# Optimization experiments

Hardware: AMD Instinct MI355X
Metric: run time of the kernel (lower is better)

Reference implementation:

```python
import math
import jax, jax.numpy as jnp
import numpy as np

B, C, T = 4, 512, 1024
H = 8
KC = C // H
WIN = 4


def _get_relative_embeddings(emb, length):
    win = (emb.shape[1] - 1) // 2
    pad_length = max(length - (win + 1), 0)
    slice_start = max(win + 1 - length, 0)
    slice_end = slice_start + 2 * length - 1
    if pad_length > 0:
        emb = jnp.pad(emb, ((0, 0), (pad_length, pad_length), (0, 0)))
    return emb[:, slice_start:slice_end]


def _relative_to_absolute(x):
    # x: [b, h, L, 2L-1] -> [b, h, L, L] via skew trick
    b, h, L, _ = x.shape
    x = jnp.pad(x, ((0, 0), (0, 0), (0, 0), (0, 1)))          # [b,h,L,2L]
    x_flat = x.reshape(b, h, L * 2 * L)
    x_flat = jnp.pad(x_flat, ((0, 0), (0, 0), (0, L - 1)))    # [b,h,(L+1)(2L-1)]
    x_final = x_flat.reshape(b, h, L + 1, 2 * L - 1)
    return x_final[:, :, :L, L - 1:]


def _absolute_to_relative(x):
    # x: [b, h, L, L] -> [b, h, L, 2L-1]
    b, h, L, _ = x.shape
    x = jnp.pad(x, ((0, 0), (0, 0), (0, 0), (0, L - 1)))      # [b,h,L,2L-1]
    x_flat = x.reshape(b, h, L * (2 * L - 1))
    x_flat = jnp.pad(x_flat, ((0, 0), (0, 0), (L, 0)))        # [b,h,2L^2]
    x_final = x_flat.reshape(b, h, L, 2 * L)
    return x_final[:, :, :, 1:]


def setup_inputs() -> dict:
    key = jax.random.key(0)
    ks = jax.random.split(key, 12)
    xavier = math.sqrt(6.0 / (C + C))  # xavier_uniform for [C, C, 1] conv weight
    rel_std = KC ** (-0.5)
    return {
        "x": jax.random.normal(ks[0], (B, C, T), dtype=jnp.float32),
        "wq": jax.random.uniform(ks[1], (C, C), jnp.float32, -xavier, xavier),
        "bq": jnp.zeros((C,), jnp.float32),
        "wk": jax.random.uniform(ks[2], (C, C), jnp.float32, -xavier, xavier),
        "bk": jnp.zeros((C,), jnp.float32),
        "wv": jax.random.uniform(ks[3], (C, C), jnp.float32, -xavier, xavier),
        "bv": jnp.zeros((C,), jnp.float32),
        "wo": jax.random.normal(ks[4], (C, C), jnp.float32) * (1.0 / math.sqrt(C)),
        "bo": jnp.zeros((C,), jnp.float32),
        "emb_rel_k": jax.random.normal(ks[5], (1, 2 * WIN + 1, KC), jnp.float32) * rel_std,
        "emb_rel_v": jax.random.normal(ks[6], (1, 2 * WIN + 1, KC), jnp.float32) * rel_std,
    }


def reference(x, wq, bq, wk, bk, wv, bv, wo, bo, emb_rel_k, emb_rel_v):
    b, c, t = x.shape
    # 1x1 conv == channel matmul
    q = jnp.einsum("oi,bit->bot", wq, x) + bq[:, None]
    k = jnp.einsum("oi,bit->bot", wk, x) + bk[:, None]
    v = jnp.einsum("oi,bit->bot", wv, x) + bv[:, None]
    # [b, H, t, kc]
    q = q.reshape(b, H, KC, t).transpose(0, 1, 3, 2)
    k = k.reshape(b, H, KC, t).transpose(0, 1, 3, 2)
    v = v.reshape(b, H, KC, t).transpose(0, 1, 3, 2)
    inv_sqrt = 1.0 / math.sqrt(KC)
    scores = jnp.einsum("bhtc,bhsc->bhts", q, k) * inv_sqrt
    rel_k = _get_relative_embeddings(emb_rel_k, t)[0]            # [2t-1, kc]
    rel_logits = jnp.einsum("bhtc,rc->bhtr", q, rel_k)           # [b,h,t,2t-1]
    scores = scores + _relative_to_absolute(rel_logits) * inv_sqrt
    p_attn = jax.nn.softmax(scores, axis=-1)
    output = jnp.einsum("bhts,bhsc->bhtc", p_attn, v)
    rel_weights = _absolute_to_relative(p_attn)                  # [b,h,t,2t-1]
    rel_v = _get_relative_embeddings(emb_rel_v, t)[0]            # [2t-1, kc]
    output = output + jnp.einsum("bhtr,rc->bhtc", rel_weights, rel_v)
    output = output.transpose(0, 1, 3, 2).reshape(b, c, t)
    return jnp.einsum("oi,bit->bot", wo, output) + bo[:, None]
```

## Files before the change

### kernel.cpp

```cpp
#include <hip/hip_runtime.h>
#include <hip/hip_bf16.h>

#define Bdim 4
#define Cdim 512
#define Tdim 1024
#define Hn   8
#define KCd  64

typedef __attribute__((ext_vector_type(8))) short bf16x8;
typedef __attribute__((ext_vector_type(4))) float f32x4;

__device__ __forceinline__ unsigned short f32_bf16_rne(float f) {
    unsigned u = __float_as_uint(f);
    u += 0x7FFFu + ((u >> 16) & 1u);
    return (unsigned short)(u >> 16);
}
__device__ __forceinline__ float bf16_f32(unsigned short h) {
    return __uint_as_float(((unsigned)h) << 16);
}
__device__ __forceinline__ void split8(const float* f, bf16x8& h8, bf16x8& l8) {
    #pragma unroll
    for (int e = 0; e < 8; ++e) {
        const unsigned short hh = f32_bf16_rne(f[e]);
        h8[e] = (short)hh;
        l8[e] = (short)f32_bf16_rne(f[e] - bf16_f32(hh));
    }
}

__device__ __forceinline__ int sw(int row, int col) {
    return (row << 6) + ((((col >> 3) ^ (row & 7)) << 3) | (col & 7));
}
__device__ __forceinline__ bf16x8 fragld(const unsigned short* a, int row, int kstep, int quad) {
    return *(const bf16x8*)&a[(row << 6) + ((((kstep << 2) | quad) ^ (row & 7)) << 3)];
}


__global__ __launch_bounds__(256) void prep_kernel(
    const float* __restrict__ wq, const float* __restrict__ wk,
    const float* __restrict__ wv, const float* __restrict__ wo,
    const float* __restrict__ x,
    unsigned short* __restrict__ WAhi, unsigned short* __restrict__ WAlo,
    unsigned short* __restrict__ XBhi, unsigned short* __restrict__ XBlo)
{
    const int w = threadIdx.x >> 6, lane = threadIdx.x & 63;
    const int l15 = lane & 15, quad = lane >> 4;
    const int task = blockIdx.x * 4 + w;

    if (task < 2048) {
        const int mtile = task >> 4, kt = task & 15;
        const int sel = mtile >> 5;
        const float* W = sel == 0 ? wq : (sel == 1 ? wk : (sel == 2 ? wv : wo));
        const int row = (mtile & 31) * 16 + l15;
        const float* p = W + (size_t)row * Cdim + kt * 32 + quad * 8;
        float f[8];
        *(float4*)&f[0] = *(const float4*)p;
        *(float4*)&f[4] = *(const float4*)(p + 4);
        bf16x8 h8, l8;
        split8(f, h8, l8);
        const size_t base = (size_t)task * 512 + lane * 8;
        *(bf16x8*)(WAhi + base) = h8;
        *(bf16x8*)(WAlo + base) = l8;
    } else {
        const int t2 = task - 2048;
        const int b = t2 >> 10, ntile = (t2 >> 4) & 63, kt = t2 & 15;
        const float* Xb = x + (size_t)b * Cdim * Tdim;
        const int n = ntile * 16 + l15;
        const int k0 = kt * 32 + quad * 8;
        float f[8];
        #pragma unroll
        for (int e = 0; e < 8; ++e) f[e] = Xb[(size_t)(k0 + e) * Tdim + n];
        bf16x8 h8, l8;
        split8(f, h8, l8);
        const size_t base = (size_t)t2 * 512 + lane * 8;
        *(bf16x8*)(XBhi + base) = h8;
        *(bf16x8*)(XBlo + base) = l8;
    }
}

__global__ __launch_bounds__(256, 3) void gemm_qkv(
    const unsigned short* __restrict__ Ahi, const unsigned short* __restrict__ Alo,
    const unsigned short* __restrict__ Bhi, const unsigned short* __restrict__ Blo,
    const float* __restrict__ bq, const float* __restrict__ bk, const float* __restrict__ bv,
    unsigned short* __restrict__ qhi, unsigned short* __restrict__ qlo,
    unsigned short* __restrict__ khi, unsigned short* __restrict__ klo,
    unsigned short* __restrict__ vhi, unsigned short* __restrict__ vlo)
{
    const int tid = threadIdx.x;
    const int w = tid >> 6, lane = tid & 63;
    const int l15 = lane & 15, quad = lane >> 4;
    const int lo8 = lane << 3;

    const int id = blockIdx.x;
    const int xcd = id & 7, slot = id >> 3;
    const int col = xcd * 16 + slot / 6;
    const int mg  = slot % 6;
    const int b = col >> 5, n32 = col & 31;
    const int m64 = mg * 4 + w;
    const int sel = m64 >> 3;
    const int mtb = m64 * 4;
    const int ntb = b * 64 + n32 * 2;

    f32x4 acc[4][2];
    #pragma unroll
    for (int i = 0; i < 4; ++i)
        #pragma unroll
        for (int j = 0; j < 2; ++j) acc[i][j] = (f32x4){0.f, 0.f, 0.f, 0.f};

    bf16x8 Ah[2][4], Al[2][4], Bh[2][2], Bl[2][2];
    #pragma unroll
    for (int mt = 0; mt < 4; ++mt) {
        const size_t o = (size_t)(mtb + mt) * 8192 + lo8;
        Ah[0][mt] = *(const bf16x8*)(Ahi + o);
        Al[0][mt] = *(const bf16x8*)(Alo + o);
    }
    #pragma unroll
    for (int nt = 0; nt < 2; ++nt) {
        const size_t o = (size_t)(ntb + nt) * 8192 + lo8;
        Bh[0][nt] = *(const bf16x8*)(Bhi + o);
        Bl[0][nt] = *(const bf16x8*)(Blo + o);
    }

    for (int kt = 0; kt < 16; ++kt) {
        const int cur = kt & 1, nxt = cur ^ 1;
        if (kt < 15) {
            const int kn = (kt + 1) * 512;
            #pragma unroll
            for (int mt = 0; mt < 4; ++mt) {
                const size_t o = (size_t)(mtb + mt) * 8192 + kn + lo8;
                Ah[nxt][mt] = *(const bf16x8*)(Ahi + o);
                Al[nxt][mt] = *(const bf16x8*)(Alo + o);
            }
            #pragma unroll
            for (int nt = 0; nt < 2; ++nt) {
                const size_t o = (size_t)(ntb + nt) * 8192 + kn + lo8;
                Bh[nxt][nt] = *(const bf16x8*)(Bhi + o);
                Bl[nxt][nt] = *(const bf16x8*)(Blo + o);
            }
        }
        #pragma unroll
        for (int mt = 0; mt < 4; ++mt)
            #pragma unroll
            for (int nt = 0; nt < 2; ++nt) {
                f32x4 c = acc[mt][nt];
                c = __builtin_amdgcn_mfma_f32_16x16x32_bf16(Ah[cur][mt], Bh[cur][nt], c, 0, 0, 0);
                c = __builtin_amdgcn_mfma_f32_16x16x32_bf16(Ah[cur][mt], Bl[cur][nt], c, 0, 0, 0);
                c = __builtin_amdgcn_mfma_f32_16x16x32_bf16(Al[cur][mt], Bh[cur][nt], c, 0, 0, 0);
                acc[mt][nt] = c;
            }
    }

    const int head = m64 & 7;
    const size_t hbase = ((size_t)(b * Hn + head) * 16) << 12;
    if (sel < 2) {
        const float* Bv = sel == 0 ? bq : bk;
        unsigned short* ph = sel == 0 ? qhi : khi;
        unsigned short* pl = sel == 0 ? qlo : klo;
        #pragma unroll
        for (int mt = 0; mt < 4; ++mt) {
            const int c0 = mt * 16 + quad * 4;
            float bb[4];
            #pragma unroll
            for (int r = 0; r < 4; ++r) bb[r] = Bv[head * 64 + c0 + r];
            const int lane_out = (((c0 >> 3) & 3) << 4) + l15;
            const int e0 = c0 & 7;
            const int cg = c0 >> 5;
            #pragma unroll
            for (int nt = 0; nt < 2; ++nt) {
                const int tile = n32 >> 1;
                const int rhi = (n32 & 1) * 2 + nt;
                const int g = rhi * 2 + cg;
                const size_t off = hbase + ((size_t)tile << 12) + g * 512
                                 + (size_t)lane_out * 8 + e0;
                ushort4 h4, l4;
                #pragma unroll
                for (int r = 0; r < 4; ++r) {
                    const float v = acc[mt][nt][r] + bb[r];
                    const unsigned short hh = f32_bf16_rne(v);
                    ((unsigned short*)&h4)[r] = hh;
                    ((unsigned short*)&l4)[r] = f32_bf16_rne(v - bf16_f32(hh));
                }
                *(ushort4*)(ph + off) = h4;
                *(ushort4*)(pl + off) = l4;
            }
        }
    } else {
        #pragma unroll
        for (int mt = 0; mt < 4; ++mt) {
            const int c0 = mt * 16 + quad * 4;
            float bb[4];
            #pragma unroll
            for (int r = 0; r < 4; ++r) bb[r] = bv[head * 64 + c0 + r];
            #pragma unroll
            for (int nt = 0; nt < 2; ++nt) {
                const int t = n32 * 32 + nt * 16 + l15;
                const int tile = t >> 6, jl = t & 63;
                const int jg = jl >> 5, lanej = ((jl >> 3) & 3) << 4;
                const int e = jl & 7;
                const size_t tb = hbase + ((size_t)tile << 12);
                #pragma unroll
                for (int r = 0; r < 4; ++r) {
                    const int c = c0 + r;
                    const int g = mt * 2 + jg;
                    const int lane_v = lanej + (c & 15);
                    const float v = acc[mt][nt][r] + bb[r];
                    const unsigned short hh = f32_bf16_rne(v);
                    const size_t off = tb + g * 512 + (size_t)lane_v * 8 + e;
                    vhi[off] = hh;
                    vlo[off] = f32_bf16_rne(v - bf16_f32(hh));
                }
            }
        }
    }
}

__global__ __launch_bounds__(256) void gemm_out(
    const unsigned short* __restrict__ Ahi, const unsigned short* __restrict__ Alo,
    const unsigned short* __restrict__ Bhi, const unsigned short* __restrict__ Blo,
    const float* __restrict__ bo, float* __restrict__ out)
{
    const int tid = threadIdx.x;
    const int w = tid >> 6, lane = tid & 63;
    const int l15 = lane & 15, quad = lane >> 4;
    const int lo8 = lane << 3;

    const int id = blockIdx.x;
    const int xcd = id & 7, slot = id >> 3;
    const int col = xcd * 16 + (slot >> 2);
    const int mg  = slot & 3;
    const int b = col >> 5, n32 = col & 31;
    const int m32 = mg * 4 + w;
    const int mtb = 96 + m32 * 2;
    const int ntb = b * 64 + n32 * 2;

    f32x4 acc[2][2];
    #pragma unroll
    for (int i = 0; i < 2; ++i)
        #pragma unroll
        for (int j = 0; j < 2; ++j) acc[i][j] = (f32x4){0.f, 0.f, 0.f, 0.f};

    bf16x8 Ah[2][2], Al[2][2], Bh[2][2], Bl[2][2];
    #pragma unroll
    for (int mt = 0; mt < 2; ++mt) {
        const size_t o = (size_t)(mtb + mt) * 8192 + lo8;
        Ah[0][mt] = *(const bf16x8*)(Ahi + o);
        Al[0][mt] = *(const bf16x8*)(Alo + o);
    }
    #pragma unroll
    for (int nt = 0; nt < 2; ++nt) {
        const size_t o = (size_t)(ntb + nt) * 8192 + lo8;
        Bh[0][nt] = *(const bf16x8*)(Bhi + o);
        Bl[0][nt] = *(const bf16x8*)(Blo + o);
    }

    for (int kt = 0; kt < 16; ++kt) {
        const int cur = kt & 1, nxt = cur ^ 1;
        if (kt < 15) {
            const int kn = (kt + 1) * 512;
            #pragma unroll
            for (int mt = 0; mt < 2; ++mt) {
                const size_t o = (size_t)(mtb + mt) * 8192 + kn + lo8;
                Ah[nxt][mt] = *(const bf16x8*)(Ahi + o);
                Al[nxt][mt] = *(const bf16x8*)(Alo + o);
            }
            #pragma unroll
            for (int nt = 0; nt < 2; ++nt) {
                const size_t o = (size_t)(ntb + nt) * 8192 + kn + lo8;
                Bh[nxt][nt] = *(const bf16x8*)(Bhi + o);
                Bl[nxt][nt] = *(const bf16x8*)(Blo + o);
            }
        }
        #pragma unroll
        for (int mt = 0; mt < 2; ++mt)
            #pragma unroll
            for (int nt = 0; nt < 2; ++nt) {
                f32x4 c = acc[mt][nt];
                c = __builtin_amdgcn_mfma_f32_16x16x32_bf16(Ah[cur][mt], Bh[cur][nt], c, 0, 0, 0);
                c = __builtin_amdgcn_mfma_f32_16x16x32_bf16(Ah[cur][mt], Bl[cur][nt], c, 0, 0, 0);
                c = __builtin_amdgcn_mfma_f32_16x16x32_bf16(Al[cur][mt], Bh[cur][nt], c, 0, 0, 0);
                acc[mt][nt] = c;
            }
    }

    float* Ob = out + (size_t)b * Cdim * Tdim;
    #pragma unroll
    for (int mt = 0; mt < 2; ++mt) {
        const int m = m32 * 32 + mt * 16 + quad * 4;
        float bb[4];
        #pragma unroll
        for (int r = 0; r < 4; ++r) bb[r] = bo[m + r];
        #pragma unroll
        for (int nt = 0; nt < 2; ++nt) {
            const int t = n32 * 32 + nt * 16 + l15;
            #pragma unroll
            for (int r = 0; r < 4; ++r)
                Ob[(size_t)(m + r) * Tdim + t] = acc[mt][nt][r] + bb[r];
        }
    }
}

__global__ __launch_bounds__(256) void attn_mfma(
    const unsigned short* __restrict__ qhi, const unsigned short* __restrict__ qlo,
    const unsigned short* __restrict__ khi, const unsigned short* __restrict__ klo,
    const unsigned short* __restrict__ vhi, const unsigned short* __restrict__ vlo,
    const float* __restrict__ ek,
    const float* __restrict__ ev,
    unsigned short* __restrict__ cxhi, unsigned short* __restrict__ cxlo)
{
    __shared__ alignas(16) unsigned short psh[4096], psl[4096];
    __shared__ float rk[576];
    __shared__ float evs[576];

    const int tid = threadIdx.x;
    int it, h, b;
    {
        const int n = blockIdx.x;
        const int xcd = n & 7, slot = n >> 3;
        const int pair = (xcd << 2) | (slot >> 4);
        it = slot & 15;
        b = pair >> 3;
        h = pair & 7;
    }
    const int i0 = it * 64;
    const int lane = tid & 63, w = tid >> 6;
    const int l15 = lane & 15, quad = lane >> 4;
    const int m_blk = w * 16 + l15;
    const int lo8 = lane << 3;

    const size_t bh16 = (size_t)(b * Hn + h) * 16;

    bf16x8 qfh[2], qfl[2];
    {
        const unsigned short* qth = qhi + ((bh16 + it) << 12);
        const unsigned short* qtl = qlo + ((bh16 + it) << 12);
        #pragma unroll
        for (int ks = 0; ks < 2; ++ks) {
            qfh[ks] = *(const bf16x8*)(qth + (((w << 1) | ks) << 9) + lo8);
            qfl[ks] = *(const bf16x8*)(qtl + (((w << 1) | ks) << 9) + lo8);
        }
    }

    bf16x8 ekh[2], ekl[2];
    #pragma unroll
    for (int ks = 0; ks < 2; ++ks) {
        #pragma unroll
        for (int j = 0; j < 8; ++j) { ekh[ks][j] = 0; ekl[ks][j] = 0; }
        if (l15 < 9) {
            #pragma unroll
            for (int j = 0; j < 8; ++j) {
                const float v = ek[l15 * 64 + ks * 32 + quad * 8 + j];
                const unsigned short hh = f32_bf16_rne(v);
                ekh[ks][j] = (short)hh;
                ekl[ks][j] = (short)f32_bf16_rne(v - bf16_f32(hh));
            }
        }
    }

    {
        f32x4 rkD = (f32x4){0.f, 0.f, 0.f, 0.f};
        #pragma unroll
        for (int ks = 0; ks < 2; ++ks) {
            rkD = __builtin_amdgcn_mfma_f32_16x16x32_bf16(qfh[ks], ekh[ks], rkD, 0, 0, 0);
            rkD = __builtin_amdgcn_mfma_f32_16x16x32_bf16(qfh[ks], ekl[ks], rkD, 0, 0, 0);
            rkD = __builtin_amdgcn_mfma_f32_16x16x32_bf16(qfl[ks], ekh[ks], rkD, 0, 0, 0);
        }
        if (l15 < 9) {
            #pragma unroll
            for (int r = 0; r < 4; ++r)
                rk[(w * 16 + quad * 4 + r) * 9 + l15] = rkD[r];
        }
    }
    for (int idx = tid; idx < 576; idx += 256) evs[idx] = ev[idx];
    __syncthreads();

    float m_run = -1e30f, l_run = 0.f;
    f32x4 Oc[4];
    #pragma unroll
    for (int ct = 0; ct < 4; ++ct) Oc[ct] = (f32x4){0.f, 0.f, 0.f, 0.f};

    const unsigned short* kh0 = khi + (bh16 << 12);
    const unsigned short* kl0 = klo + (bh16 << 12);
    const unsigned short* vh0 = vhi + (bh16 << 12);
    const unsigned short* vl0 = vlo + (bh16 << 12);

    for (int t = 0; t < 16; ++t) {
        const int j0 = t << 6;
        const size_t tb = (size_t)t << 12;
        const unsigned short* kht = kh0 + tb;
        const unsigned short* klt = kl0 + tb;
        const unsigned short* vht = vh0 + tb;
        const unsigned short* vlt = vl0 + tb;

        bf16x8 vbh[2][4], vbl[2][4];
        #pragma unroll
        for (int ks = 0; ks < 2; ++ks)
            #pragma unroll
            for (int ct = 0; ct < 4; ++ct) {
                vbh[ks][ct] = *(const bf16x8*)(vht + (((ct << 1) | ks) << 9) + lo8);
                vbl[ks][ct] = *(const bf16x8*)(vlt + (((ct << 1) | ks) << 9) + lo8);
            }

        f32x4 Sc[4];
        #pragma unroll
        for (int jt = 0; jt < 4; ++jt) Sc[jt] = (f32x4){0.f, 0.f, 0.f, 0.f};
        #pragma unroll
        for (int ks = 0; ks < 2; ++ks) {
            bf16x8 ah[4], al[4];
            #pragma unroll
            for (int jt = 0; jt < 4; ++jt) {
                ah[jt] = *(const bf16x8*)(kht + (((jt << 1) | ks) << 9) + lo8);
                al[jt] = *(const bf16x8*)(klt + (((jt << 1) | ks) << 9) + lo8);
            }
            #pragma unroll
            for (int jt = 0; jt < 4; ++jt) {
                Sc[jt] = __builtin_amdgcn_mfma_f32_16x16x32_bf16(ah[jt], qfh[ks], Sc[jt], 0, 0, 0);
                Sc[jt] = __builtin_amdgcn_mfma_f32_16x16x32_bf16(ah[jt], qfl[ks], Sc[jt], 0, 0, 0);
                Sc[jt] = __builtin_amdgcn_mfma_f32_16x16x32_bf16(al[jt], qfh[ks], Sc[jt], 0, 0, 0);
            }
        }

        const int dt = j0 - i0;
        const bool diag = (dt >= -67 && dt <= 67);
        if (diag) {
            #pragma unroll
            for (int jt = 0; jt < 4; ++jt) {
                const int db = dt + jt * 16 + quad * 4 - m_blk;
                #pragma unroll
                for (int r = 0; r < 4; ++r) {
                    const int d = db + r;
                    if ((unsigned)(d + 4) <= 8u) Sc[jt][r] += rk[m_blk * 9 + d + 4];
                }
            }
        }

        float mt = -1e30f;
        #pragma unroll
        for (int jt = 0; jt < 4; ++jt)
            #pragma unroll
            for (int r = 0; r < 4; ++r) {
                Sc[jt][r] *= 0.125f;
                mt = fmaxf(mt, Sc[jt][r]);
            }
        mt = fmaxf(mt, __shfl_xor(mt, 16));
        mt = fmaxf(mt, __shfl_xor(mt, 32));
        const float mn = fmaxf(m_run, mt);
        const float alpha = __expf(m_run - mn);
        float rs = 0.f;
        #pragma unroll
        for (int jt = 0; jt < 4; ++jt)
            #pragma unroll
            for (int r = 0; r < 4; ++r) {
                const float e = __expf(Sc[jt][r] - mn);
                Sc[jt][r] = e;
                rs += e;
            }
        rs += __shfl_xor(rs, 16);
        rs += __shfl_xor(rs, 32);
        l_run = l_run * alpha + rs;
        m_run = mn;

        #pragma unroll
        for (int jt = 0; jt < 4; ++jt) {
            ushort4 ph, pl;
            ph.x = f32_bf16_rne(Sc[jt][0]); pl.x = f32_bf16_rne(Sc[jt][0] - bf16_f32(ph.x));
            ph.y = f32_bf16_rne(Sc[jt][1]); pl.y = f32_bf16_rne(Sc[jt][1] - bf16_f32(ph.y));
            ph.z = f32_bf16_rne(Sc[jt][2]); pl.z = f32_bf16_rne(Sc[jt][2] - bf16_f32(ph.z));
            ph.w = f32_bf16_rne(Sc[jt][3]); pl.w = f32_bf16_rne(Sc[jt][3] - bf16_f32(ph.w));
            const int o = sw(m_blk, jt * 16 + quad * 4);
            *(ushort4*)&psh[o] = ph;
            *(ushort4*)&psl[o] = pl;
        }

        const float al0 = __shfl(alpha, quad * 4 + 0);
        const float al1 = __shfl(alpha, quad * 4 + 1);
        const float al2 = __shfl(alpha, quad * 4 + 2);
        const float al3 = __shfl(alpha, quad * 4 + 3);
        #pragma unroll
        for (int ct = 0; ct < 4; ++ct) {
            Oc[ct][0] *= al0; Oc[ct][1] *= al1; Oc[ct][2] *= al2; Oc[ct][3] *= al3;
        }
        #pragma unroll
        for (int ks = 0; ks < 2; ++ks) {
            bf16x8 pah = fragld(psh, m_blk, ks, quad);
            bf16x8 pal = fragld(psl, m_blk, ks, quad);
            #pragma unroll
            for (int ct = 0; ct < 4; ++ct) {
                Oc[ct] = __builtin_amdgcn_mfma_f32_16x16x32_bf16(pah, vbh[ks][ct], Oc[ct], 0, 0, 0);
                Oc[ct] = __builtin_amdgcn_mfma_f32_16x16x32_bf16(pah, vbl[ks][ct], Oc[ct], 0, 0, 0);
                Oc[ct] = __builtin_amdgcn_mfma_f32_16x16x32_bf16(pal, vbh[ks][ct], Oc[ct], 0, 0, 0);
            }
        }

        if (diag) {
            #pragma unroll
            for (int r = 0; r < 4; ++r) {
                const int mrow = w * 16 + quad * 4 + r;
                const int ig = i0 + mrow;
                #pragma unroll
                for (int e = 0; e < 9; ++e) {
                    const int jl = ig + e - 4 - j0;
                    if ((unsigned)jl < 64u) {
                        const int o = sw(mrow, jl);
                        const float p = bf16_f32(psh[o]) + bf16_f32(psl[o]);
                        #pragma unroll
                        for (int ct = 0; ct < 4; ++ct)
                            Oc[ct][r] += p * evs[e * 64 + ct * 16 + l15];
                    }
                }
            }
        }
    }

    const float rlv = 1.f / l_run;
    float rl[4];
    rl[0] = __shfl(rlv, quad * 4 + 0);
    rl[1] = __shfl(rlv, quad * 4 + 1);
    rl[2] = __shfl(rlv, quad * 4 + 2);
    rl[3] = __shfl(rlv, quad * 4 + 3);
    const int ntile16 = it * 4 + w;
    const int e = l15 & 7;
    #pragma unroll
    for (int ct = 0; ct < 4; ++ct) {
        const int cl = ct * 16 + l15;
        const int ktc = h * 2 + (cl >> 5);
        const int lane_c = (((ct * 2 + (l15 >> 3)) & 3) << 4) + quad * 4;
        const size_t base = (((size_t)(b * 64 + ntile16)) * 16 + ktc) * 512;
        #pragma unroll
        for (int r = 0; r < 4; ++r) {
            const float v = Oc[ct][r] * rl[r];
            const unsigned short hh = f32_bf16_rne(v);
            const size_t off = base + (size_t)(lane_c + r) * 8 + e;
            cxhi[off] = hh;
            cxlo[off] = f32_bf16_rne(v - bf16_f32(hh));
        }
    }
}

extern "C" void kernel_launch(void* const* d_in, const int* in_sizes, int n_in,
                              void* d_out, int out_size, void* d_ws, size_t ws_size,
                              hipStream_t stream) {
    const float* x  = (const float*)d_in[0];
    const float* wq = (const float*)d_in[1];
    const float* bq = (const float*)d_in[2];
    const float* wk = (const float*)d_in[3];
    const float* bk = (const float*)d_in[4];
    const float* wv = (const float*)d_in[5];
    const float* bv = (const float*)d_in[6];
    const float* wo = (const float*)d_in[7];
    const float* bo = (const float*)d_in[8];
    const float* ek = (const float*)d_in[9];
    const float* ev = (const float*)d_in[10];
    float* out = (float*)d_out;

    const size_t PW = 2048u * 512u;
    const size_t PX = 4u * 1024u * 512u;
    unsigned short* WAhi = (unsigned short*)d_ws;
    unsigned short* WAlo = WAhi + PW;
    unsigned short* XBhi = WAlo + PW;
    unsigned short* XBlo = XBhi + PX;
    unsigned short* qhi  = XBlo + PX;
    unsigned short* qlo  = qhi + PX;
    unsigned short* khi  = qlo + PX;
    unsigned short* klo  = khi + PX;
    unsigned short* vhi  = klo + PX;
    unsigned short* vlo  = vhi + PX;
    unsigned short* cxhi = vlo + PX;
    unsigned short* cxlo = cxhi + PX;

    prep_kernel<<<dim3(1536), 256, 0, stream>>>(
        wq, wk, wv, wo, x, WAhi, WAlo, XBhi, XBlo);

    gemm_qkv<<<dim3(768), 256, 0, stream>>>(
        WAhi, WAlo, XBhi, XBlo, bq, bk, bv,
        qhi, qlo, khi, klo, vhi, vlo);

    attn_mfma<<<dim3(512), 256, 0, stream>>>(
        qhi, qlo, khi, klo, vhi, vlo, ek, ev, cxhi, cxlo);

    gemm_out<<<dim3(512), 256, 0, stream>>>(
        WAhi, WAlo, cxhi, cxlo, bo, out);
}
```

Baseline: 181.9 us.

## Use packed bf16 conversion, exp2 softmax, skip-rescale, and register-held band probabilities

Replaces the software round-to-nearest bf16 split with the hardware v_cvt_pk_bf16_f32 packed conversion in all kernels. Folds the log2(e) factor into the score scale so raw v_exp_f32 can be used, and skips the output rescale when no row max grows. The relative-value band now reads exact fp32 probabilities from a small shared buffer instead of reconstructing them from the hi/lo tiles, with the ev embeddings held in registers. This cuts ALU work in the softmax and conversion paths, at the cost of more registers and an extra shared-memory band buffer whose write and read ordering needs care.

```diff
diff --git a/kernel.cpp b/kernel.cpp
--- a/kernel.cpp
+++ b/kernel.cpp
@@ -18,13 +18,35 @@
 __device__ __forceinline__ float bf16_f32(unsigned short h) {
     return __uint_as_float(((unsigned)h) << 16);
 }
+
+__device__ __forceinline__ unsigned pk2(float a, float b) {
+    unsigned r;
+    asm("v_cvt_pk_bf16_f32 %0, %1, %2" : "=v"(r) : "v"(a), "v"(b));
+    return r;
+}
+__device__ __forceinline__ float exp2_fast(float x) {
+    float r;
+    asm("v_exp_f32 %0, %1" : "=v"(r) : "v"(x));
+    return r;
+}
+__device__ __forceinline__ void split4_pk(float v0, float v1, float v2, float v3,
+                                          unsigned& h01, unsigned& h23,
+                                          unsigned& l01, unsigned& l23) {
+    h01 = pk2(v0, v1);
+    h23 = pk2(v2, v3);
+    const float r0 = v0 - __uint_as_float(h01 << 16);
+    const float r1 = v1 - __uint_as_float(h01 & 0xffff0000u);
+    const float r2 = v2 - __uint_as_float(h23 << 16);
+    const float r3 = v3 - __uint_as_float(h23 & 0xffff0000u);
+    l01 = pk2(r0, r1);
+    l23 = pk2(r2, r3);
+}
 __device__ __forceinline__ void split8(const float* f, bf16x8& h8, bf16x8& l8) {
-    #pragma unroll
-    for (int e = 0; e < 8; ++e) {
-        const unsigned short hh = f32_bf16_rne(f[e]);
-        h8[e] = (short)hh;
-        l8[e] = (short)f32_bf16_rne(f[e] - bf16_f32(hh));
-    }
+    union U { bf16x8 v; unsigned u[4]; };
+    U H, L;
+    split4_pk(f[0], f[1], f[2], f[3], H.u[0], H.u[1], L.u[0], L.u[1]);
+    split4_pk(f[4], f[5], f[6], f[7], H.u[2], H.u[3], L.u[2], L.u[3]);
+    h8 = H.v; l8 = L.v;
 }
 
 __device__ __forceinline__ int sw(int row, int col) {
@@ -171,16 +193,14 @@
                 const int g = rhi * 2 + cg;
                 const size_t off = hbase + ((size_t)tile << 12) + g * 512
                                  + (size_t)lane_out * 8 + e0;
-                ushort4 h4, l4;
-                #pragma unroll
-                for (int r = 0; r < 4; ++r) {
-                    const float v = acc[mt][nt][r] + bb[r];
-                    const unsigned short hh = f32_bf16_rne(v);
-                    ((unsigned short*)&h4)[r] = hh;
-                    ((unsigned short*)&l4)[r] = f32_bf16_rne(v - bf16_f32(hh));
-                }
-                *(ushort4*)(ph + off) = h4;
-                *(ushort4*)(pl + off) = l4;
+                unsigned h01, h23, l01, l23;
+                split4_pk(acc[mt][nt][0] + bb[0], acc[mt][nt][1] + bb[1],
+                          acc[mt][nt][2] + bb[2], acc[mt][nt][3] + bb[3],
+                          h01, h23, l01, l23);
+                uint2 hv; hv.x = h01; hv.y = h23;
+                uint2 lv; lv.x = l01; lv.y = l23;
+                *(uint2*)(ph + off) = hv;
+                *(uint2*)(pl + off) = lv;
             }
         }
     } else {
@@ -197,16 +217,20 @@
                 const int jg = jl >> 5, lanej = ((jl >> 3) & 3) << 4;
                 const int e = jl & 7;
                 const size_t tb = hbase + ((size_t)tile << 12);
+                unsigned h01, h23, l01, l23;
+                split4_pk(acc[mt][nt][0] + bb[0], acc[mt][nt][1] + bb[1],
+                          acc[mt][nt][2] + bb[2], acc[mt][nt][3] + bb[3],
+                          h01, h23, l01, l23);
                 #pragma unroll
                 for (int r = 0; r < 4; ++r) {
                     const int c = c0 + r;
                     const int g = mt * 2 + jg;
                     const int lane_v = lanej + (c & 15);
-                    const float v = acc[mt][nt][r] + bb[r];
-                    const unsigned short hh = f32_bf16_rne(v);
                     const size_t off = tb + g * 512 + (size_t)lane_v * 8 + e;
-                    vhi[off] = hh;
-                    vlo[off] = f32_bf16_rne(v - bf16_f32(hh));
+                    const unsigned hw = (r & 2) ? h23 : h01;
+                    const unsigned lw = (r & 2) ? l23 : l01;
+                    vhi[off] = (unsigned short)(hw >> ((r & 1) * 16));
+                    vlo[off] = (unsigned short)(lw >> ((r & 1) * 16));
                 }
             }
         }
@@ -308,7 +332,9 @@
 {
     __shared__ alignas(16) unsigned short psh[4096], psl[4096];
     __shared__ float rk[576];
-    __shared__ float evs[576];
+    __shared__ float bandp[576];
+
+    const float SCALE = 0.125f * 1.44269504088896f;
 
     const int tid = threadIdx.x;
     int it, h, b;
@@ -366,11 +392,16 @@
         if (l15 < 9) {
             #pragma unroll
             for (int r = 0; r < 4; ++r)
-                rk[(w * 16 + quad * 4 + r) * 9 + l15] = rkD[r];
-        }
-    }
-    for (int idx = tid; idx < 576; idx += 256) evs[idx] = ev[idx];
-    __syncthreads();
+                rk[(w * 16 + quad * 4 + r) * 9 + l15] = rkD[r] * SCALE;
+        }
+    }
+
+    float evr[9][4];
+    #pragma unroll
+    for (int e = 0; e < 9; ++e)
+        #pragma unroll
+        for (int ct = 0; ct < 4; ++ct)
+            evr[e][ct] = ev[e * 64 + ct * 16 + l15];
 
     float m_run = -1e30f, l_run = 0.f;
     f32x4 Oc[4];
@@ -418,6 +449,11 @@
             }
         }
 
+        #pragma unroll
+        for (int jt = 0; jt < 4; ++jt)
+            #pragma unroll
+            for (int r = 0; r < 4; ++r) Sc[jt][r] *= SCALE;
+
         const int dt = j0 - i0;
         const bool diag = (dt >= -67 && dt <= 67);
         if (diag) {
@@ -432,52 +468,68 @@
             }
         }
 
-        float mt = -1e30f;
+        const float mt = fmaxf(
+            fmaxf(fmaxf(fmaxf(Sc[0][0], Sc[0][1]), fmaxf(Sc[0][2], Sc[0][3])),
+                  fmaxf(fmaxf(Sc[1][0], Sc[1][1]), fmaxf(Sc[1][2], Sc[1][3]))),
+            fmaxf(fmaxf(fmaxf(Sc[2][0], Sc[2][1]), fmaxf(Sc[2][2], Sc[2][3])),
+                  fmaxf(fmaxf(Sc[3][0], Sc[3][1]), fmaxf(Sc[3][2], Sc[3][3]))));
+        float mr = fmaxf(mt, __shfl_xor(mt, 16));
+        mr = fmaxf(mr, __shfl_xor(mr, 32));
+        const float mn = fmaxf(m_run, mr);
+
         #pragma unroll
         for (int jt = 0; jt < 4; ++jt)
             #pragma unroll
-            for (int r = 0; r < 4; ++r) {
-                Sc[jt][r] *= 0.125f;
-                mt = fmaxf(mt, Sc[jt][r]);
-            }
-        mt = fmaxf(mt, __shfl_xor(mt, 16));
-        mt = fmaxf(mt, __shfl_xor(mt, 32));
-        const float mn = fmaxf(m_run, mt);
-        const float alpha = __expf(m_run - mn);
-        float rs = 0.f;
-        #pragma unroll
-        for (int jt = 0; jt < 4; ++jt)
-            #pragma unroll
-            for (int r = 0; r < 4; ++r) {
-                const float e = __expf(Sc[jt][r] - mn);
-                Sc[jt][r] = e;
-                rs += e;
-            }
+            for (int r = 0; r < 4; ++r)
+                Sc[jt][r] = exp2_fast(Sc[jt][r] - mn);
+
+        float rs = ((Sc[0][0] + Sc[0][1]) + (Sc[0][2] + Sc[0][3]))
+                 + ((Sc[1][0] + Sc[1][1]) + (Sc[1][2] + Sc[1][3]))
+                 + ((Sc[2][0] + Sc[2][1]) + (Sc[2][2] + Sc[2][3]))
+                 + ((Sc[3][0] + Sc[3][1]) + (Sc[3][2] + Sc[3][3]));
         rs += __shfl_xor(rs, 16);
         rs += __shfl_xor(rs, 32);
+
+        const bool grow = __any(mr > m_run);
+        float alpha = 1.f;
+        if (grow) alpha = exp2_fast(m_run - mn);
         l_run = l_run * alpha + rs;
         m_run = mn;
 
+        if (diag) {
+            #pragma unroll
+            for (int jt = 0; jt < 4; ++jt) {
+                const int db = dt + jt * 16 + quad * 4 - m_blk;
+                #pragma unroll
+                for (int r = 0; r < 4; ++r) {
+                    const int d = db + r;
+                    if ((unsigned)(d + 4) <= 8u) bandp[m_blk * 9 + d + 4] = Sc[jt][r];
+                }
+            }
+        }
+
         #pragma unroll
         for (int jt = 0; jt < 4; ++jt) {
-            ushort4 ph, pl;
-            ph.x = f32_bf16_rne(Sc[jt][0]); pl.x = f32_bf16_rne(Sc[jt][0] - bf16_f32(ph.x));
-            ph.y = f32_bf16_rne(Sc[jt][1]); pl.y = f32_bf16_rne(Sc[jt][1] - bf16_f32(ph.y));
-            ph.z = f32_bf16_rne(Sc[jt][2]); pl.z = f32_bf16_rne(Sc[jt][2] - bf16_f32(ph.z));
-            ph.w = f32_bf16_rne(Sc[jt][3]); pl.w = f32_bf16_rne(Sc[jt][3] - bf16_f32(ph.w));
+            unsigned h01, h23, l01, l23;
+            split4_pk(Sc[jt][0], Sc[jt][1], Sc[jt][2], Sc[jt][3], h01, h23, l01, l23);
             const int o = sw(m_blk, jt * 16 + quad * 4);
-            *(ushort4*)&psh[o] = ph;
-            *(ushort4*)&psl[o] = pl;
-        }
-
-        const float al0 = __shfl(alpha, quad * 4 + 0);
-        const float al1 = __shfl(alpha, quad * 4 + 1);
-        const float al2 = __shfl(alpha, quad * 4 + 2);
-        const float al3 = __shfl(alpha, quad * 4 + 3);
-        #pragma unroll
-        for (int ct = 0; ct < 4; ++ct) {
-            Oc[ct][0] *= al0; Oc[ct][1] *= al1; Oc[ct][2] *= al2; Oc[ct][3] *= al3;
-        }
+            uint2 hv; hv.x = h01; hv.y = h23;
+            uint2 lv; lv.x = l01; lv.y = l23;
+            *(uint2*)&psh[o] = hv;
+            *(uint2*)&psl[o] = lv;
+        }
+
+        if (grow) {
+            const float al0 = __shfl(alpha, quad * 4 + 0);
+            const float al1 = __shfl(alpha, quad * 4 + 1);
+            const float al2 = __shfl(alpha, quad * 4 + 2);
+            const float al3 = __shfl(alpha, quad * 4 + 3);
+            #pragma unroll
+            for (int ct = 0; ct < 4; ++ct) {
+                Oc[ct][0] *= al0; Oc[ct][1] *= al1; Oc[ct][2] *= al2; Oc[ct][3] *= al3;
+            }
+        }
+
         #pragma unroll
         for (int ks = 0; ks < 2; ++ks) {
             bf16x8 pah = fragld(psh, m_blk, ks, quad);
@@ -499,11 +551,10 @@
                 for (int e = 0; e < 9; ++e) {
                     const int jl = ig + e - 4 - j0;
                     if ((unsigned)jl < 64u) {
-                        const int o = sw(mrow, jl);
-                        const float p = bf16_f32(psh[o]) + bf16_f32(psl[o]);
+                        const float p = bandp[mrow * 9 + e];
                         #pragma unroll
                         for (int ct = 0; ct < 4; ++ct)
-                            Oc[ct][r] += p * evs[e * 64 + ct * 16 + l15];
+                            Oc[ct][r] += p * evr[e][ct];
                     }
                 }
             }
@@ -524,13 +575,16 @@
         const int ktc = h * 2 + (cl >> 5);
         const int lane_c = (((ct * 2 + (l15 >> 3)) & 3) << 4) + quad * 4;
         const size_t base = (((size_t)(b * 64 + ntile16)) * 16 + ktc) * 512;
+        unsigned h01, h23, l01, l23;
+        split4_pk(Oc[ct][0] * rl[0], Oc[ct][1] * rl[1],
+                  Oc[ct][2] * rl[2], Oc[ct][3] * rl[3], h01, h23, l01, l23);
         #pragma unroll
         for (int r = 0; r < 4; ++r) {
-            const float v = Oc[ct][r] * rl[r];
-            const unsigned short hh = f32_bf16_rne(v);
             const size_t off = base + (size_t)(lane_c + r) * 8 + e;
-            cxhi[off] = hh;
-            cxlo[off] = f32_bf16_rne(v - bf16_f32(hh));
+            const unsigned hw = (r & 2) ? h23 : h01;
+            const unsigned lw = (r & 2) ? l23 : l01;
+            cxhi[off] = (unsigned short)(hw >> ((r & 1) * 16));
+            cxlo[off] = (unsigned short)(lw >> ((r & 1) * 16));
         }
     }
 }
```

After: 209.8 us. 1.15x slower.
